# Optimization experiments

Hardware: AMD Instinct MI355X
Metric: run time of the kernel (lower is better)

The kernel has to match this reference:

```python
import jax, jax.numpy as jnp
import numpy as np

N, T, DS, DA = 256, 64, 32, 8
D, H, FF = 512, 8, 2048
HD = D // H          # head_dim = 64
IN = DS + DA         # input_dim = 40
EULER_STEPS = 4


def setup_inputs():
    key = jax.random.key(0)
    ks = jax.random.split(key, 12)
    g = lambda k, shape: (jax.random.normal(k, shape) * 0.02).astype(jnp.float32)
    z = lambda *s: jnp.zeros(s, jnp.float32)
    o = lambda *s: jnp.ones(s, jnp.float32)
    return {
        "states": jax.random.normal(ks[0], (N, T, DS), jnp.float32),
        "actions": jax.random.normal(ks[1], (N, T, DA), jnp.float32),
        "time_steps": jnp.cumsum(jax.random.uniform(ks[2], (N, T + 1), jnp.float32, 0.01, 0.1), axis=1),
        "W_ode": g(ks[3], (D, D)), "b_ode": z(D),
        "W_in": g(ks[4], (IN, D)), "b_in": z(D),
        "ln_in_g": o(D), "ln_in_b": z(D),
        "W_q": g(ks[5], (D, D)), "b_q": z(D),
        "W_kv": g(ks[6], (IN + D, 2 * D + H)), "b_kv": z(2 * D + H),
        "W_out": g(ks[7], (D, D)), "b_out": z(D),
        "ln_ff_g": o(D), "ln_ff_b": z(D),
        "W_ff1": g(ks[8], (D, FF)), "b_ff1": z(FF),
        "W_ff2": g(ks[9], (FF, D)), "b_ff2": z(D),
        "W_dec": g(ks[10], (D, DS)), "b_dec": z(DS),
    }


def _ln(x, g, b):
    m = jnp.mean(x, -1, keepdims=True)
    v = jnp.mean((x - m) ** 2, -1, keepdims=True)
    return (x - m) * jax.lax.rsqrt(v + 1e-5) * g + b


def _forward(states, actions, time_steps, W_ode, b_ode, W_in, b_in, ln_in_g, ln_in_b,
             W_q, b_q, W_kv, b_kv, W_out, b_out, ln_ff_g, ln_ff_b,
             W_ff1, b_ff1, W_ff2, b_ff2, W_dec, b_dec):
    n = states.shape[0]
    # teacher forcing path (train=True, eps_decay=0): data_i = cat(states_i, actions_i)
    data_seq = jnp.concatenate([states, actions], -1).transpose(1, 0, 2)  # [T, N, IN]
    dts = (time_steps[:, 1:] - time_steps[:, :-1]).T                      # [T, N]

    def step(carry, xs):
        h1, W2 = carry            # h1: [N, D], W2: [N, H, HD, HD] fast weights
        data, dt = xs
        # integrate latent ODE over per-sample dt (fixed-step Euler, autonomous tanh MLP)
        step_dt = (dt / EULER_STEPS)[:, None]
        for _ in range(EULER_STEPS):
            h1 = h1 + step_dt * jnp.tanh(h1 @ W_ode + b_ode)
        # Hebbian fast-weight update: W2 += lr * v (x) k  (per head)
        x = jnp.concatenate([data, h1], -1)
        kvb = x @ W_kv + b_kv
        k = jax.nn.softmax(kvb[:, :D].reshape(n, H, HD), -1)
        v = jnp.tanh(kvb[:, D:2 * D]).reshape(n, H, HD)
        lr = jax.nn.sigmoid(kvb[:, 2 * D:])                    # [N, H]
        W2 = W2 + lr[:, :, None, None] * jnp.einsum('nhv,nhk->nhvk', v, k)
        # query_fast_weight
        q = _ln(data @ W_in + b_in, ln_in_g, ln_in_b) @ W_q + b_q
        q = jax.nn.softmax(q.reshape(n, H, HD), -1)
        out = jnp.einsum('nhvk,nhk->nhv', W2, q).reshape(n, D)
        out = out @ W_out + b_out
        y = _ln(out, ln_ff_g, ln_ff_b)
        out = jnp.maximum(y @ W_ff1 + b_ff1, 0.0) @ W_ff2 + b_ff2 + out  # FF block + residual
        pred = out @ W_dec + b_dec                              # decoder
        return (out, W2), pred

    h0 = jnp.zeros((n, D), states.dtype)
    W20 = jnp.zeros((n, H, HD, HD), states.dtype)
    _, preds = jax.lax.scan(step, (h0, W20), (data_seq, dts))
    return preds.transpose(1, 0, 2)  # [N, T, DS] predicted next states


def reference(states, actions, time_steps, W_ode, b_ode, W_in, b_in, ln_in_g, ln_in_b,
              W_q, b_q, W_kv, b_kv, W_out, b_out, ln_ff_g, ln_ff_b,
              W_ff1, b_ff1, W_ff2, b_ff2, W_dec, b_dec):
    return _forward(states, actions, time_steps, W_ode, b_ode, W_in, b_in, ln_in_g, ln_in_b,
                    W_q, b_q, W_kv, b_kv, W_out, b_out, ln_ff_g, ln_ff_b,
                    W_ff1, b_ff1, W_ff2, b_ff2, W_dec, b_dec)
```

## Files before the change

### kernel.cpp

```cpp
#include <hip/hip_runtime.h>

#define NS   256
#define TS   64
#define DS   32
#define DA   8
#define DD   512
#define HH   8
#define HD   64
#define FF   2048
#define INP  40
#define INPP 20
#define INPG 24
#define DP   256
#define KVKP 276
#define KVKPP 280
#define KVO  1032
#define FFP  1024

#define OFF_ODE 0
#define SZ_ODE  (32*512*8)
#define OFF_KV  (OFF_ODE+SZ_ODE)
#define SZ_KV   (35*1032*8)
#define OFF_IN  (OFF_KV+SZ_KV)
#define SZ_IN   (3*512*8)
#define OFF_Q   (OFF_IN+SZ_IN)
#define SZ_Q    (32*512*8)
#define OFF_OUT (OFF_Q+SZ_Q)
#define SZ_OUT  (32*512*8)
#define OFF_F1  (OFF_OUT+SZ_OUT)
#define SZ_F1   (32*2048*8)
#define OFF_F2  (OFF_F1+SZ_F1)
#define SZ_F2   (128*512*8)
#define OFF_DEC (OFF_F2+SZ_F2)
#define SZ_DEC  (32*32*8)

#define DEV __device__ __forceinline__

typedef _Float16 half2_t __attribute__((ext_vector_type(2)));

DEV half2_t as_h2(unsigned int u) { return __builtin_bit_cast(half2_t, u); }

DEV float dot2f(unsigned int w, unsigned int x, float acc) {
#if __has_builtin(__builtin_amdgcn_fdot2)
  return __builtin_amdgcn_fdot2(as_h2(w), as_h2(x), acc, false);
#else
  half2_t a = as_h2(w), b = as_h2(x);
  return acc + (float)a[0] * (float)b[0] + (float)a[1] * (float)b[1];
#endif
}

DEV unsigned int pack2f(float a, float b) {
  unsigned short ua = __builtin_bit_cast(unsigned short, (_Float16)a);
  unsigned short ub = __builtin_bit_cast(unsigned short, (_Float16)b);
  return ((unsigned int)ub << 16) | (unsigned int)ua;
}

DEV float fast_tanh(float x) {
  float ax = fabsf(x);
  float e  = __expf(-2.0f * ax);
  float r  = (1.0f - e) / (1.0f + e);
  return copysignf(r, x);
}

DEV float fast_sigmoid(float x) { return 1.0f / (1.0f + __expf(-x)); }

DEV float wave_max(float v) {
  #pragma unroll
  for (int o = 32; o; o >>= 1) v = fmaxf(v, __shfl_xor(v, o));
  return v;
}
DEV float wave_sum(float v) {
  #pragma unroll
  for (int o = 32; o; o >>= 1) v += __shfl_xor(v, o);
  return v;
}

DEV float dotG(const unsigned int* __restrict__ Wc, int strideG,
               const unsigned int* __restrict__ xq, int NG, float init) {
  float a0 = init, a1 = 0.f, a2 = 0.f, a3 = 0.f;
  #pragma unroll 4
  for (int g = 0; g < NG; ++g) {
    uint4 w0 = *reinterpret_cast<const uint4*>(Wc + g * strideG);
    uint4 w1 = *reinterpret_cast<const uint4*>(Wc + g * strideG + 4);
    uint4 x0 = *reinterpret_cast<const uint4*>(xq + g * 8);
    uint4 x1 = *reinterpret_cast<const uint4*>(xq + g * 8 + 4);
    a0 = dot2f(w0.x, x0.x, a0);
    a1 = dot2f(w0.y, x0.y, a1);
    a2 = dot2f(w0.z, x0.z, a2);
    a3 = dot2f(w0.w, x0.w, a3);
    a0 = dot2f(w1.x, x1.x, a0);
    a1 = dot2f(w1.y, x1.y, a1);
    a2 = dot2f(w1.z, x1.z, a2);
    a3 = dot2f(w1.w, x1.w, a3);
  }
  return (a0 + a1) + (a2 + a3);
}

__global__ void pack_wg_kernel(const float* __restrict__ src, unsigned int* __restrict__ dst,
                               int K, int KPpad, int Dout) {
  int idx = blockIdx.x * blockDim.x + threadIdx.x;
  int total = KPpad * Dout;
  if (idx >= total) return;
  int kp = idx / Dout;
  int j  = idx - kp * Dout;
  int r0 = 2 * kp, r1 = r0 + 1;
  float lo = (r0 < K) ? src[r0 * Dout + j] : 0.f;
  float hi = (r1 < K) ? src[r1 * Dout + j] : 0.f;
  int kg = kp >> 3, sub = kp & 7;
  dst[((kg * Dout + j) << 3) + sub] = pack2f(lo, hi);
}

__global__ __launch_bounds__(512) void fwp_main(
    const float* __restrict__ states, const float* __restrict__ actions,
    const float* __restrict__ tsteps,
    const float* __restrict__ b_ode, const float* __restrict__ b_in,
    const float* __restrict__ ln_in_g, const float* __restrict__ ln_in_b,
    const float* __restrict__ b_q, const float* __restrict__ b_kv,
    const float* __restrict__ b_out,
    const float* __restrict__ ln_ff_g, const float* __restrict__ ln_ff_b,
    const float* __restrict__ b_ff1, const float* __restrict__ b_ff2,
    const float* __restrict__ b_dec,
    const unsigned int* __restrict__ Wode, const unsigned int* __restrict__ Wkv,
    const unsigned int* __restrict__ Win,  const unsigned int* __restrict__ Wq,
    const unsigned int* __restrict__ Wout, const unsigned int* __restrict__ Wff1,
    const unsigned int* __restrict__ Wff2, const unsigned int* __restrict__ Wdec,
    unsigned int* __restrict__ ctrs, float* __restrict__ outp) {

  const int n = blockIdx.x, tid = threadIdx.x;
  const int w = tid >> 6, lane = tid & 63;

  __shared__ alignas(16) float        sh_h[DD];
  __shared__ alignas(16) unsigned int sh_hp[DP];
  __shared__ alignas(16) unsigned int sh_xp[KVKPP];
  __shared__ alignas(16) unsigned int sh_dp[INPG];
  __shared__ alignas(16) float        sh_t[DD];
  __shared__ alignas(16) unsigned int sh_p[DP];
  __shared__ alignas(16) float        sh_kvb[KVO];
  __shared__ alignas(16) float        sh_k[DD];
  __shared__ alignas(16) float        sh_v[DD];
  __shared__ alignas(16) float        sh_q[DD];
  __shared__ float                    sh_lr[HH];
  __shared__ alignas(16) float        sh_ff[FF];
  __shared__ alignas(16) unsigned int sh_ffp[FFP];
  __shared__ float                    sh_red[16];
  __shared__ alignas(16) float        sh_decp[512];
  __shared__ int                      sh_flag;

  float W2r[64];
  #pragma unroll
  for (int i = 0; i < 64; ++i) W2r[i] = 0.f;

  sh_h[tid] = 0.f;
  if (tid < DP) sh_hp[tid] = 0u;
  if (tid >= DP && tid < DP + (KVKPP - KVKP)) sh_xp[KVKP + (tid - DP)] = 0u;
  if (tid >= 300 && tid < 300 + (INPG - INPP)) sh_dp[INPP + (tid - 300)] = 0u;

  bool pace = true;
  unsigned int* ctr = ctrs + 16 * (n & 7);

  for (int t = 0; t < TS; ++t) {
    __syncthreads();

    if (pace) {
      if (tid == 0) {
        sh_flag = 0;
        __hip_atomic_fetch_add(ctr, 1u, __ATOMIC_RELAXED, __HIP_MEMORY_SCOPE_AGENT);
        unsigned int tgt = 32u * (unsigned int)(t + 1);
        int it = 0;
        while (__hip_atomic_load(ctr, __ATOMIC_RELAXED, __HIP_MEMORY_SCOPE_AGENT) < tgt) {
          if (++it > 4096) { sh_flag = 1; break; }
          __builtin_amdgcn_s_sleep(8);
        }
      }
      __syncthreads();
      if (sh_flag) pace = false;
    }

    if (tid < INPP) {
      int i0 = 2 * tid, i1 = i0 + 1;
      float a = (i0 < DS) ? states[(n * TS + t) * DS + i0] : actions[(n * TS + t) * DA + (i0 - DS)];
      float b = (i1 < DS) ? states[(n * TS + t) * DS + i1] : actions[(n * TS + t) * DA + (i1 - DS)];
      unsigned int p = pack2f(a, b);
      sh_xp[tid] = p;
      sh_dp[tid] = p;
    }
    const float sdt = 0.25f * (tsteps[n * (TS + 1) + t + 1] - tsteps[n * (TS + 1) + t]);

    for (int e = 0; e < 4; ++e) {
      float acc = dotG(Wode + tid * 8, DD * 8, sh_hp, 32, b_ode[tid]);
      sh_h[tid] += sdt * fast_tanh(acc);
      __syncthreads();
      if (tid < DP) sh_hp[tid] = pack2f(sh_h[2 * tid], sh_h[2 * tid + 1]);
      __syncthreads();
    }

    if (tid < DP) sh_xp[INPP + tid] = sh_hp[tid];
    __syncthreads();

    for (int j = tid; j < KVO; j += 512)
      sh_kvb[j] = dotG(Wkv + j * 8, KVO * 8, sh_xp, 35, b_kv[j]);
    __syncthreads();

    {
      float kx = sh_kvb[tid];
      float km = wave_max(kx);
      float ke = __expf(kx - km);
      float ks = wave_sum(ke);
      sh_k[tid] = ke / ks;
      sh_v[tid] = fast_tanh(sh_kvb[DD + tid]);
      if (tid < HH) sh_lr[tid] = fast_sigmoid(sh_kvb[2 * DD + tid]);
    }

    float y1 = dotG(Win + tid * 8, DD * 8, sh_dp, 3, b_in[tid]);
    {
      float s1 = y1, s2 = y1 * y1;
      #pragma unroll
      for (int o = 32; o; o >>= 1) { s1 += __shfl_xor(s1, o); s2 += __shfl_xor(s2, o); }
      if (lane == 0) { sh_red[2 * w] = s1; sh_red[2 * w + 1] = s2; }
      __syncthreads();
      s1 = 0.f; s2 = 0.f;
      #pragma unroll
      for (int i = 0; i < 8; ++i) { s1 += sh_red[2 * i]; s2 += sh_red[2 * i + 1]; }
      float m  = s1 * (1.0f / DD);
      float va = fmaxf(s2 * (1.0f / DD) - m * m, 0.f);
      float rs = rsqrtf(va + 1e-5f);
      sh_t[tid] = (y1 - m) * rs * ln_in_g[tid] + ln_in_b[tid];
    }
    __syncthreads();
    if (tid < DP) sh_p[tid] = pack2f(sh_t[2 * tid], sh_t[2 * tid + 1]);
    __syncthreads();
    {
      float qraw = dotG(Wq + tid * 8, DD * 8, sh_p, 32, b_q[tid]);
      float qm = wave_max(qraw);
      float qe = __expf(qraw - qm);
      float qs = wave_sum(qe);
      sh_q[tid] = qe / qs;
    }
    __syncthreads();

    {
      float vi  = sh_v[tid];
      float lrw = sh_lr[w];
      float lv  = lrw * vi;
      float acc = 0.f;
      const float* kb = sh_k + w * HD;
      const float* qb = sh_q + w * HD;
      #pragma unroll
      for (int jc = 0; jc < 16; ++jc) {
        float4 k4 = *reinterpret_cast<const float4*>(kb + 4 * jc);
        float4 q4 = *reinterpret_cast<const float4*>(qb + 4 * jc);
        W2r[4 * jc + 0] += lv * k4.x; acc += W2r[4 * jc + 0] * q4.x;
        W2r[4 * jc + 1] += lv * k4.y; acc += W2r[4 * jc + 1] * q4.y;
        W2r[4 * jc + 2] += lv * k4.z; acc += W2r[4 * jc + 2] * q4.z;
        W2r[4 * jc + 3] += lv * k4.w; acc += W2r[4 * jc + 3] * q4.w;
      }
      sh_t[tid] = acc;
    }
    __syncthreads();
    if (tid < DP) sh_p[tid] = pack2f(sh_t[2 * tid], sh_t[2 * tid + 1]);
    __syncthreads();

    float o1 = dotG(Wout + tid * 8, DD * 8, sh_p, 32, b_out[tid]);

    {
      float s1 = o1, s2 = o1 * o1;
      #pragma unroll
      for (int o = 32; o; o >>= 1) { s1 += __shfl_xor(s1, o); s2 += __shfl_xor(s2, o); }
      if (lane == 0) { sh_red[2 * w] = s1; sh_red[2 * w + 1] = s2; }
      __syncthreads();
      s1 = 0.f; s2 = 0.f;
      #pragma unroll
      for (int i = 0; i < 8; ++i) { s1 += sh_red[2 * i]; s2 += sh_red[2 * i + 1]; }
      float m  = s1 * (1.0f / DD);
      float va = fmaxf(s2 * (1.0f / DD) - m * m, 0.f);
      float rs = rsqrtf(va + 1e-5f);
      sh_t[tid] = (o1 - m) * rs * ln_ff_g[tid] + ln_ff_b[tid];
    }
    __syncthreads();
    if (tid < DP) sh_p[tid] = pack2f(sh_t[2 * tid], sh_t[2 * tid + 1]);
    __syncthreads();

    {
      float f0 = b_ff1[tid], f1 = b_ff1[tid + 512], f2 = b_ff1[tid + 1024], f3 = b_ff1[tid + 1536];
      #pragma unroll 2
      for (int g = 0; g < 32; ++g) {
        uint4 x0 = *reinterpret_cast<const uint4*>(sh_p + g * 8);
        uint4 x1 = *reinterpret_cast<const uint4*>(sh_p + g * 8 + 4);
        const unsigned int* wb = Wff1 + g * (FF * 8) + tid * 8;
        uint4 wa0 = *reinterpret_cast<const uint4*>(wb);
        uint4 wa1 = *reinterpret_cast<const uint4*>(wb + 4);
        uint4 wb0 = *reinterpret_cast<const uint4*>(wb + 512 * 8);
        uint4 wb1 = *reinterpret_cast<const uint4*>(wb + 512 * 8 + 4);
        uint4 wc0 = *reinterpret_cast<const uint4*>(wb + 1024 * 8);
        uint4 wc1 = *reinterpret_cast<const uint4*>(wb + 1024 * 8 + 4);
        uint4 wd0 = *reinterpret_cast<const uint4*>(wb + 1536 * 8);
        uint4 wd1 = *reinterpret_cast<const uint4*>(wb + 1536 * 8 + 4);
        f0 = dot2f(wa0.x, x0.x, f0); f0 = dot2f(wa0.y, x0.y, f0);
        f0 = dot2f(wa0.z, x0.z, f0); f0 = dot2f(wa0.w, x0.w, f0);
        f0 = dot2f(wa1.x, x1.x, f0); f0 = dot2f(wa1.y, x1.y, f0);
        f0 = dot2f(wa1.z, x1.z, f0); f0 = dot2f(wa1.w, x1.w, f0);
        f1 = dot2f(wb0.x, x0.x, f1); f1 = dot2f(wb0.y, x0.y, f1);
        f1 = dot2f(wb0.z, x0.z, f1); f1 = dot2f(wb0.w, x0.w, f1);
        f1 = dot2f(wb1.x, x1.x, f1); f1 = dot2f(wb1.y, x1.y, f1);
        f1 = dot2f(wb1.z, x1.z, f1); f1 = dot2f(wb1.w, x1.w, f1);
        f2 = dot2f(wc0.x, x0.x, f2); f2 = dot2f(wc0.y, x0.y, f2);
        f2 = dot2f(wc0.z, x0.z, f2); f2 = dot2f(wc0.w, x0.w, f2);
        f2 = dot2f(wc1.x, x1.x, f2); f2 = dot2f(wc1.y, x1.y, f2);
        f2 = dot2f(wc1.z, x1.z, f2); f2 = dot2f(wc1.w, x1.w, f2);
        f3 = dot2f(wd0.x, x0.x, f3); f3 = dot2f(wd0.y, x0.y, f3);
        f3 = dot2f(wd0.z, x0.z, f3); f3 = dot2f(wd0.w, x0.w, f3);
        f3 = dot2f(wd1.x, x1.x, f3); f3 = dot2f(wd1.y, x1.y, f3);
        f3 = dot2f(wd1.z, x1.z, f3); f3 = dot2f(wd1.w, x1.w, f3);
      }
      sh_ff[tid]        = fmaxf(f0, 0.f);
      sh_ff[tid + 512]  = fmaxf(f1, 0.f);
      sh_ff[tid + 1024] = fmaxf(f2, 0.f);
      sh_ff[tid + 1536] = fmaxf(f3, 0.f);
    }
    __syncthreads();
    sh_ffp[tid]       = pack2f(sh_ff[2 * tid], sh_ff[2 * tid + 1]);
    sh_ffp[tid + 512] = pack2f(sh_ff[2 * tid + 1024], sh_ff[2 * tid + 1025]);
    __syncthreads();

    {
      float o2 = dotG(Wff2 + tid * 8, DD * 8, sh_ffp, 128, b_ff2[tid]) + o1;
      sh_h[tid] = o2;
    }
    __syncthreads();
    if (tid < DP) sh_hp[tid] = pack2f(sh_h[2 * tid], sh_h[2 * tid + 1]);
    __syncthreads();

    {
      int col = tid & 31, ch = tid >> 5;
      const unsigned int* wbse = Wdec + col * 8;
      float a = 0.f;
      #pragma unroll
      for (int g = 2 * ch; g < 2 * ch + 2; ++g) {
        uint4 w0 = *reinterpret_cast<const uint4*>(wbse + g * (DS * 8));
        uint4 w1 = *reinterpret_cast<const uint4*>(wbse + g * (DS * 8) + 4);
        uint4 x0 = *reinterpret_cast<const uint4*>(sh_hp + g * 8);
        uint4 x1 = *reinterpret_cast<const uint4*>(sh_hp + g * 8 + 4);
        a = dot2f(w0.x, x0.x, a); a = dot2f(w0.y, x0.y, a);
        a = dot2f(w0.z, x0.z, a); a = dot2f(w0.w, x0.w, a);
        a = dot2f(w1.x, x1.x, a); a = dot2f(w1.y, x1.y, a);
        a = dot2f(w1.z, x1.z, a); a = dot2f(w1.w, x1.w, a);
      }
      sh_decp[tid] = a;
    }
    __syncthreads();
    if (tid < DS) {
      float s = b_dec[tid];
      #pragma unroll
      for (int c = 0; c < 16; ++c) s += sh_decp[c * 32 + tid];
      outp[(n * TS + t) * DS + tid] = s;
    }
  }
}

extern "C" void kernel_launch(void* const* d_in, const int* in_sizes, int n_in,
                              void* d_out, int out_size, void* d_ws, size_t ws_size,
                              hipStream_t stream) {
  (void)in_sizes; (void)n_in; (void)out_size; (void)ws_size;

  const float* states   = (const float*)d_in[0];
  const float* actions  = (const float*)d_in[1];
  const float* tsteps   = (const float*)d_in[2];
  const float* W_ode    = (const float*)d_in[3];
  const float* b_ode    = (const float*)d_in[4];
  const float* W_in     = (const float*)d_in[5];
  const float* b_in     = (const float*)d_in[6];
  const float* ln_in_g  = (const float*)d_in[7];
  const float* ln_in_b  = (const float*)d_in[8];
  const float* W_q      = (const float*)d_in[9];
  const float* b_q      = (const float*)d_in[10];
  const float* W_kv     = (const float*)d_in[11];
  const float* b_kv     = (const float*)d_in[12];
  const float* W_out    = (const float*)d_in[13];
  const float* b_out    = (const float*)d_in[14];
  const float* ln_ff_g  = (const float*)d_in[15];
  const float* ln_ff_b  = (const float*)d_in[16];
  const float* W_ff1    = (const float*)d_in[17];
  const float* b_ff1    = (const float*)d_in[18];
  const float* W_ff2    = (const float*)d_in[19];
  const float* b_ff2    = (const float*)d_in[20];
  const float* W_dec    = (const float*)d_in[21];
  const float* b_dec    = (const float*)d_in[22];

  unsigned int* wsbase = (unsigned int*)d_ws;
  unsigned int* ctrs   = wsbase;
  unsigned int* W      = wsbase + 128;

  hipMemsetAsync(d_ws, 0, 512, stream);

  auto launch_pack = [&](const float* src, unsigned int* dst, int K, int KPpad, int Dout) {
    int total = KPpad * Dout;
    int blocks = (total + 255) / 256;
    pack_wg_kernel<<<blocks, 256, 0, stream>>>(src, dst, K, KPpad, Dout);
  };

  launch_pack(W_ode, W + OFF_ODE, 512,  256, 512);
  launch_pack(W_kv,  W + OFF_KV,  552,  280, 1032);
  launch_pack(W_in,  W + OFF_IN,  40,   24,  512);
  launch_pack(W_q,   W + OFF_Q,   512,  256, 512);
  launch_pack(W_out, W + OFF_OUT, 512,  256, 512);
  launch_pack(W_ff1, W + OFF_F1,  512,  256, 2048);
  launch_pack(W_ff2, W + OFF_F2,  2048, 1024, 512);
  launch_pack(W_dec, W + OFF_DEC, 512,  256, 32);

  fwp_main<<<NS, 512, 0, stream>>>(
      states, actions, tsteps,
      b_ode, b_in, ln_in_g, ln_in_b, b_q, b_kv, b_out, ln_ff_g, ln_ff_b,
      b_ff1, b_ff2, b_dec,
      W + OFF_ODE, W + OFF_KV, W + OFF_IN, W + OFF_Q,
      W + OFF_OUT, W + OFF_F1, W + OFF_F2, W + OFF_DEC,
      ctrs, (float*)d_out);
}
```

Before: 5.905 ms.

## Process two samples per block to reuse each weight load twice

Each block now handles two batch samples, so every packed weight vector fetched from global memory feeds dot products for both samples. The grid halves to 128 blocks and the pacing target is adjusted to match. This halves weight traffic per sample but doubles the fast-weight registers (128 floats per thread) and the shared memory footprint, which can cause spills, and with only 128 blocks part of the GPU's compute units sit idle.

```diff
diff --git a/kernel.cpp b/kernel.cpp
--- a/kernel.cpp
+++ b/kernel.cpp
@@ -1,6 +1,7 @@
 #include <hip/hip_runtime.h>
 
 #define NS   256
+#define NB   128
 #define TS   64
 #define DS   32
 #define DA   8
@@ -64,36 +65,32 @@
 
 DEV float fast_sigmoid(float x) { return 1.0f / (1.0f + __expf(-x)); }
 
-DEV float wave_max(float v) {
-  #pragma unroll
-  for (int o = 32; o; o >>= 1) v = fmaxf(v, __shfl_xor(v, o));
-  return v;
-}
-DEV float wave_sum(float v) {
-  #pragma unroll
-  for (int o = 32; o; o >>= 1) v += __shfl_xor(v, o);
-  return v;
-}
-
-DEV float dotG(const unsigned int* __restrict__ Wc, int strideG,
-               const unsigned int* __restrict__ xq, int NG, float init) {
-  float a0 = init, a1 = 0.f, a2 = 0.f, a3 = 0.f;
+#define LD4(p) (*reinterpret_cast<const uint4*>(p))
+
+DEV void dotG2(const unsigned int* __restrict__ Wc, int strideG,
+               const unsigned int* __restrict__ xa, const unsigned int* __restrict__ xb,
+               int NG, float inita, float initb, float& outa, float& outb) {
+  float a0 = inita, a1 = 0.f, a2 = 0.f, a3 = 0.f;
+  float b0 = initb, b1 = 0.f, b2 = 0.f, b3 = 0.f;
   #pragma unroll 4
   for (int g = 0; g < NG; ++g) {
-    uint4 w0 = *reinterpret_cast<const uint4*>(Wc + g * strideG);
-    uint4 w1 = *reinterpret_cast<const uint4*>(Wc + g * strideG + 4);
-    uint4 x0 = *reinterpret_cast<const uint4*>(xq + g * 8);
-    uint4 x1 = *reinterpret_cast<const uint4*>(xq + g * 8 + 4);
-    a0 = dot2f(w0.x, x0.x, a0);
-    a1 = dot2f(w0.y, x0.y, a1);
-    a2 = dot2f(w0.z, x0.z, a2);
-    a3 = dot2f(w0.w, x0.w, a3);
-    a0 = dot2f(w1.x, x1.x, a0);
-    a1 = dot2f(w1.y, x1.y, a1);
-    a2 = dot2f(w1.z, x1.z, a2);
-    a3 = dot2f(w1.w, x1.w, a3);
+    uint4 w0 = LD4(Wc + g * strideG);
+    uint4 w1 = LD4(Wc + g * strideG + 4);
+    uint4 xa0 = LD4(xa + g * 8);
+    uint4 xa1 = LD4(xa + g * 8 + 4);
+    uint4 xb0 = LD4(xb + g * 8);
+    uint4 xb1 = LD4(xb + g * 8 + 4);
+    a0 = dot2f(w0.x, xa0.x, a0); a1 = dot2f(w0.y, xa0.y, a1);
+    a2 = dot2f(w0.z, xa0.z, a2); a3 = dot2f(w0.w, xa0.w, a3);
+    a0 = dot2f(w1.x, xa1.x, a0); a1 = dot2f(w1.y, xa1.y, a1);
+    a2 = dot2f(w1.z, xa1.z, a2); a3 = dot2f(w1.w, xa1.w, a3);
+    b0 = dot2f(w0.x, xb0.x, b0); b1 = dot2f(w0.y, xb0.y, b1);
+    b2 = dot2f(w0.z, xb0.z, b2); b3 = dot2f(w0.w, xb0.w, b3);
+    b0 = dot2f(w1.x, xb1.x, b0); b1 = dot2f(w1.y, xb1.y, b1);
+    b2 = dot2f(w1.z, xb1.z, b2); b3 = dot2f(w1.w, xb1.w, b3);
   }
-  return (a0 + a1) + (a2 + a3);
+  outa = (a0 + a1) + (a2 + a3);
+  outb = (b0 + b1) + (b2 + b3);
 }
 
 __global__ void pack_wg_kernel(const float* __restrict__ src, unsigned int* __restrict__ dst,
@@ -110,7 +107,7 @@
   dst[((kg * Dout + j) << 3) + sub] = pack2f(lo, hi);
 }
 
-__global__ __launch_bounds__(512) void fwp_main(
+__global__ __launch_bounds__(512, 2) void fwp_main(
     const float* __restrict__ states, const float* __restrict__ actions,
     const float* __restrict__ tsteps,
     const float* __restrict__ b_ode, const float* __restrict__ b_in,
@@ -126,37 +123,38 @@
     const unsigned int* __restrict__ Wff2, const unsigned int* __restrict__ Wdec,
     unsigned int* __restrict__ ctrs, float* __restrict__ outp) {
 
-  const int n = blockIdx.x, tid = threadIdx.x;
+  const int b = blockIdx.x, tid = threadIdx.x;
   const int w = tid >> 6, lane = tid & 63;
-
-  __shared__ alignas(16) float        sh_h[DD];
-  __shared__ alignas(16) unsigned int sh_hp[DP];
-  __shared__ alignas(16) unsigned int sh_xp[KVKPP];
-  __shared__ alignas(16) unsigned int sh_dp[INPG];
-  __shared__ alignas(16) float        sh_t[DD];
-  __shared__ alignas(16) unsigned int sh_p[DP];
-  __shared__ alignas(16) float        sh_kvb[KVO];
-  __shared__ alignas(16) float        sh_k[DD];
-  __shared__ alignas(16) float        sh_v[DD];
-  __shared__ alignas(16) float        sh_q[DD];
-  __shared__ float                    sh_lr[HH];
-  __shared__ alignas(16) float        sh_ff[FF];
-  __shared__ alignas(16) unsigned int sh_ffp[FFP];
-  __shared__ float                    sh_red[16];
-  __shared__ alignas(16) float        sh_decp[512];
+  const int n0 = 2 * b;
+
+  __shared__ alignas(16) float        sh_h[2][DD];
+  __shared__ alignas(16) unsigned int sh_hp[2][DP];
+  __shared__ alignas(16) unsigned int sh_xp[2][KVKPP];
+  __shared__ alignas(16) unsigned int sh_dp[2][INPG];
+  __shared__ alignas(16) float        sh_t[2][DD];
+  __shared__ alignas(16) unsigned int sh_p[2][DP];
+  __shared__ alignas(16) float        sh_kvb[2][KVO];
+  __shared__ alignas(16) float        sh_k[2][DD];
+  __shared__ alignas(16) float        sh_v[2][DD];
+  __shared__ alignas(16) float        sh_q[2][DD];
+  __shared__ float                    sh_lr[2][HH];
+  __shared__ alignas(16) float        sh_ff[2][FF];
+  __shared__ alignas(16) unsigned int sh_ffp[2][FFP];
+  __shared__ float                    sh_red[2][16];
+  __shared__ alignas(16) float        sh_decp[2][512];
   __shared__ int                      sh_flag;
 
-  float W2r[64];
+  float W2A[64], W2B[64];
   #pragma unroll
-  for (int i = 0; i < 64; ++i) W2r[i] = 0.f;
-
-  sh_h[tid] = 0.f;
-  if (tid < DP) sh_hp[tid] = 0u;
-  if (tid >= DP && tid < DP + (KVKPP - KVKP)) sh_xp[KVKP + (tid - DP)] = 0u;
-  if (tid >= 300 && tid < 300 + (INPG - INPP)) sh_dp[INPP + (tid - 300)] = 0u;
+  for (int i = 0; i < 64; ++i) { W2A[i] = 0.f; W2B[i] = 0.f; }
+
+  sh_h[0][tid] = 0.f; sh_h[1][tid] = 0.f;
+  if (tid < DP) { sh_hp[0][tid] = 0u; sh_hp[1][tid] = 0u; }
+  if (tid < (KVKPP - KVKP)) { sh_xp[0][KVKP + tid] = 0u; sh_xp[1][KVKP + tid] = 0u; }
+  if (tid < (INPG - INPP))  { sh_dp[0][INPP + tid] = 0u; sh_dp[1][INPP + tid] = 0u; }
 
   bool pace = true;
-  unsigned int* ctr = ctrs + 16 * (n & 7);
+  unsigned int* ctr = ctrs + 16 * (b & 7);
 
   for (int t = 0; t < TS; ++t) {
     __syncthreads();
@@ -165,7 +163,7 @@
       if (tid == 0) {
         sh_flag = 0;
         __hip_atomic_fetch_add(ctr, 1u, __ATOMIC_RELAXED, __HIP_MEMORY_SCOPE_AGENT);
-        unsigned int tgt = 32u * (unsigned int)(t + 1);
+        unsigned int tgt = 16u * (unsigned int)(t + 1);
         int it = 0;
         while (__hip_atomic_load(ctr, __ATOMIC_RELAXED, __HIP_MEMORY_SCOPE_AGENT) < tgt) {
           if (++it > 4096) { sh_flag = 1; break; }
@@ -176,183 +174,271 @@
       if (sh_flag) pace = false;
     }
 
-    if (tid < INPP) {
-      int i0 = 2 * tid, i1 = i0 + 1;
+    if (w < 2 && lane < INPP) {
+      int n = n0 + w;
+      int i0 = 2 * lane, i1 = i0 + 1;
       float a = (i0 < DS) ? states[(n * TS + t) * DS + i0] : actions[(n * TS + t) * DA + (i0 - DS)];
-      float b = (i1 < DS) ? states[(n * TS + t) * DS + i1] : actions[(n * TS + t) * DA + (i1 - DS)];
-      unsigned int p = pack2f(a, b);
-      sh_xp[tid] = p;
-      sh_dp[tid] = p;
-    }
-    const float sdt = 0.25f * (tsteps[n * (TS + 1) + t + 1] - tsteps[n * (TS + 1) + t]);
+      float c = (i1 < DS) ? states[(n * TS + t) * DS + i1] : actions[(n * TS + t) * DA + (i1 - DS)];
+      unsigned int p = pack2f(a, c);
+      sh_xp[w][lane] = p;
+      sh_dp[w][lane] = p;
+    }
+    const float sdtA = 0.25f * (tsteps[n0 * (TS + 1) + t + 1] - tsteps[n0 * (TS + 1) + t]);
+    const float sdtB = 0.25f * (tsteps[(n0 + 1) * (TS + 1) + t + 1] - tsteps[(n0 + 1) * (TS + 1) + t]);
 
     for (int e = 0; e < 4; ++e) {
-      float acc = dotG(Wode + tid * 8, DD * 8, sh_hp, 32, b_ode[tid]);
-      sh_h[tid] += sdt * fast_tanh(acc);
+      float accA, accB;
+      float bo = b_ode[tid];
+      dotG2(Wode + tid * 8, DD * 8, sh_hp[0], sh_hp[1], 32, bo, bo, accA, accB);
+      sh_h[0][tid] += sdtA * fast_tanh(accA);
+      sh_h[1][tid] += sdtB * fast_tanh(accB);
       __syncthreads();
-      if (tid < DP) sh_hp[tid] = pack2f(sh_h[2 * tid], sh_h[2 * tid + 1]);
+      if (tid < DP) {
+        sh_hp[0][tid] = pack2f(sh_h[0][2 * tid], sh_h[0][2 * tid + 1]);
+        sh_hp[1][tid] = pack2f(sh_h[1][2 * tid], sh_h[1][2 * tid + 1]);
+      }
       __syncthreads();
     }
 
-    if (tid < DP) sh_xp[INPP + tid] = sh_hp[tid];
-    __syncthreads();
-
-    for (int j = tid; j < KVO; j += 512)
-      sh_kvb[j] = dotG(Wkv + j * 8, KVO * 8, sh_xp, 35, b_kv[j]);
-    __syncthreads();
-
-    {
-      float kx = sh_kvb[tid];
-      float km = wave_max(kx);
+    if (tid < DP) {
+      sh_xp[0][INPP + tid] = sh_hp[0][tid];
+      sh_xp[1][INPP + tid] = sh_hp[1][tid];
+    }
+    __syncthreads();
+
+    for (int j = tid; j < KVO; j += 512) {
+      float ra, rb, bk = b_kv[j];
+      dotG2(Wkv + j * 8, KVO * 8, sh_xp[0], sh_xp[1], 35, bk, bk, ra, rb);
+      sh_kvb[0][j] = ra; sh_kvb[1][j] = rb;
+    }
+    __syncthreads();
+
+    #pragma unroll
+    for (int s = 0; s < 2; ++s) {
+      float kx = sh_kvb[s][tid];
+      float km = kx;
+      #pragma unroll
+      for (int o = 32; o; o >>= 1) km = fmaxf(km, __shfl_xor(km, o));
       float ke = __expf(kx - km);
-      float ks = wave_sum(ke);
-      sh_k[tid] = ke / ks;
-      sh_v[tid] = fast_tanh(sh_kvb[DD + tid]);
-      if (tid < HH) sh_lr[tid] = fast_sigmoid(sh_kvb[2 * DD + tid]);
-    }
-
-    float y1 = dotG(Win + tid * 8, DD * 8, sh_dp, 3, b_in[tid]);
-    {
-      float s1 = y1, s2 = y1 * y1;
-      #pragma unroll
-      for (int o = 32; o; o >>= 1) { s1 += __shfl_xor(s1, o); s2 += __shfl_xor(s2, o); }
-      if (lane == 0) { sh_red[2 * w] = s1; sh_red[2 * w + 1] = s2; }
+      float ks = ke;
+      #pragma unroll
+      for (int o = 32; o; o >>= 1) ks += __shfl_xor(ks, o);
+      sh_k[s][tid] = ke / ks;
+      sh_v[s][tid] = fast_tanh(sh_kvb[s][DD + tid]);
+      if (tid < HH) sh_lr[s][tid] = fast_sigmoid(sh_kvb[s][2 * DD + tid]);
+    }
+
+    float y1A, y1B;
+    {
+      float bi = b_in[tid];
+      dotG2(Win + tid * 8, DD * 8, sh_dp[0], sh_dp[1], 3, bi, bi, y1A, y1B);
+      float s1A = y1A, s2A = y1A * y1A, s1B = y1B, s2B = y1B * y1B;
+      #pragma unroll
+      for (int o = 32; o; o >>= 1) {
+        s1A += __shfl_xor(s1A, o); s2A += __shfl_xor(s2A, o);
+        s1B += __shfl_xor(s1B, o); s2B += __shfl_xor(s2B, o);
+      }
+      if (lane == 0) {
+        sh_red[0][2 * w] = s1A; sh_red[0][2 * w + 1] = s2A;
+        sh_red[1][2 * w] = s1B; sh_red[1][2 * w + 1] = s2B;
+      }
       __syncthreads();
-      s1 = 0.f; s2 = 0.f;
-      #pragma unroll
-      for (int i = 0; i < 8; ++i) { s1 += sh_red[2 * i]; s2 += sh_red[2 * i + 1]; }
-      float m  = s1 * (1.0f / DD);
-      float va = fmaxf(s2 * (1.0f / DD) - m * m, 0.f);
-      float rs = rsqrtf(va + 1e-5f);
-      sh_t[tid] = (y1 - m) * rs * ln_in_g[tid] + ln_in_b[tid];
-    }
-    __syncthreads();
-    if (tid < DP) sh_p[tid] = pack2f(sh_t[2 * tid], sh_t[2 * tid + 1]);
-    __syncthreads();
-    {
-      float qraw = dotG(Wq + tid * 8, DD * 8, sh_p, 32, b_q[tid]);
-      float qm = wave_max(qraw);
-      float qe = __expf(qraw - qm);
-      float qs = wave_sum(qe);
-      sh_q[tid] = qe / qs;
-    }
-    __syncthreads();
-
-    {
-      float vi  = sh_v[tid];
-      float lrw = sh_lr[w];
-      float lv  = lrw * vi;
-      float acc = 0.f;
-      const float* kb = sh_k + w * HD;
-      const float* qb = sh_q + w * HD;
+      float t1A = 0.f, t2A = 0.f, t1B = 0.f, t2B = 0.f;
+      #pragma unroll
+      for (int i = 0; i < 8; ++i) {
+        t1A += sh_red[0][2 * i]; t2A += sh_red[0][2 * i + 1];
+        t1B += sh_red[1][2 * i]; t2B += sh_red[1][2 * i + 1];
+      }
+      float mA = t1A * (1.0f / DD), mB = t1B * (1.0f / DD);
+      float vA = fmaxf(t2A * (1.0f / DD) - mA * mA, 0.f);
+      float vB = fmaxf(t2B * (1.0f / DD) - mB * mB, 0.f);
+      float rA = rsqrtf(vA + 1e-5f), rB = rsqrtf(vB + 1e-5f);
+      float g = ln_in_g[tid], bb = ln_in_b[tid];
+      sh_t[0][tid] = (y1A - mA) * rA * g + bb;
+      sh_t[1][tid] = (y1B - mB) * rB * g + bb;
+    }
+    __syncthreads();
+    if (tid < DP) {
+      sh_p[0][tid] = pack2f(sh_t[0][2 * tid], sh_t[0][2 * tid + 1]);
+      sh_p[1][tid] = pack2f(sh_t[1][2 * tid], sh_t[1][2 * tid + 1]);
+    }
+    __syncthreads();
+    {
+      float qA, qB, bq = b_q[tid];
+      dotG2(Wq + tid * 8, DD * 8, sh_p[0], sh_p[1], 32, bq, bq, qA, qB);
+      float mA = qA, mB = qB;
+      #pragma unroll
+      for (int o = 32; o; o >>= 1) { mA = fmaxf(mA, __shfl_xor(mA, o)); mB = fmaxf(mB, __shfl_xor(mB, o)); }
+      float eA = __expf(qA - mA), eB = __expf(qB - mB);
+      float sA = eA, sB = eB;
+      #pragma unroll
+      for (int o = 32; o; o >>= 1) { sA += __shfl_xor(sA, o); sB += __shfl_xor(sB, o); }
+      sh_q[0][tid] = eA / sA;
+      sh_q[1][tid] = eB / sB;
+    }
+    __syncthreads();
+
+    {
+      float lvA = sh_lr[0][w] * sh_v[0][tid];
+      float lvB = sh_lr[1][w] * sh_v[1][tid];
+      float accA = 0.f, accB = 0.f;
+      const float* kbA = sh_k[0] + w * HD;
+      const float* qbA = sh_q[0] + w * HD;
+      const float* kbB = sh_k[1] + w * HD;
+      const float* qbB = sh_q[1] + w * HD;
       #pragma unroll
       for (int jc = 0; jc < 16; ++jc) {
-        float4 k4 = *reinterpret_cast<const float4*>(kb + 4 * jc);
-        float4 q4 = *reinterpret_cast<const float4*>(qb + 4 * jc);
-        W2r[4 * jc + 0] += lv * k4.x; acc += W2r[4 * jc + 0] * q4.x;
-        W2r[4 * jc + 1] += lv * k4.y; acc += W2r[4 * jc + 1] * q4.y;
-        W2r[4 * jc + 2] += lv * k4.z; acc += W2r[4 * jc + 2] * q4.z;
-        W2r[4 * jc + 3] += lv * k4.w; acc += W2r[4 * jc + 3] * q4.w;
-      }
-      sh_t[tid] = acc;
-    }
-    __syncthreads();
-    if (tid < DP) sh_p[tid] = pack2f(sh_t[2 * tid], sh_t[2 * tid + 1]);
-    __syncthreads();
-
-    float o1 = dotG(Wout + tid * 8, DD * 8, sh_p, 32, b_out[tid]);
-
-    {
-      float s1 = o1, s2 = o1 * o1;
-      #pragma unroll
-      for (int o = 32; o; o >>= 1) { s1 += __shfl_xor(s1, o); s2 += __shfl_xor(s2, o); }
-      if (lane == 0) { sh_red[2 * w] = s1; sh_red[2 * w + 1] = s2; }
+        float4 kA = *reinterpret_cast<const float4*>(kbA + 4 * jc);
+        float4 qA = *reinterpret_cast<const float4*>(qbA + 4 * jc);
+        float4 kB = *reinterpret_cast<const float4*>(kbB + 4 * jc);
+        float4 qB = *reinterpret_cast<const float4*>(qbB + 4 * jc);
+        W2A[4 * jc + 0] += lvA * kA.x; accA += W2A[4 * jc + 0] * qA.x;
+        W2A[4 * jc + 1] += lvA * kA.y; accA += W2A[4 * jc + 1] * qA.y;
+        W2A[4 * jc + 2] += lvA * kA.z; accA += W2A[4 * jc + 2] * qA.z;
+        W2A[4 * jc + 3] += lvA * kA.w; accA += W2A[4 * jc + 3] * qA.w;
+        W2B[4 * jc + 0] += lvB * kB.x; accB += W2B[4 * jc + 0] * qB.x;
+        W2B[4 * jc + 1] += lvB * kB.y; accB += W2B[4 * jc + 1] * qB.y;
+        W2B[4 * jc + 2] += lvB * kB.z; accB += W2B[4 * jc + 2] * qB.z;
+        W2B[4 * jc + 3] += lvB * kB.w; accB += W2B[4 * jc + 3] * qB.w;
+      }
+      sh_t[0][tid] = accA;
+      sh_t[1][tid] = accB;
+    }
+    __syncthreads();
+    if (tid < DP) {
+      sh_p[0][tid] = pack2f(sh_t[0][2 * tid], sh_t[0][2 * tid + 1]);
+      sh_p[1][tid] = pack2f(sh_t[1][2 * tid], sh_t[1][2 * tid + 1]);
+    }
+    __syncthreads();
+
+    float o1A, o1B;
+    {
+      float bo = b_out[tid];
+      dotG2(Wout + tid * 8, DD * 8, sh_p[0], sh_p[1], 32, bo, bo, o1A, o1B);
+    }
+
+    {
+      float s1A = o1A, s2A = o1A * o1A, s1B = o1B, s2B = o1B * o1B;
+      #pragma unroll
+      for (int o = 32; o; o >>= 1) {
+        s1A += __shfl_xor(s1A, o); s2A += __shfl_xor(s2A, o);
+        s1B += __shfl_xor(s1B, o); s2B += __shfl_xor(s2B, o);
+      }
+      if (lane == 0) {
+        sh_red[0][2 * w] = s1A; sh_red[0][2 * w + 1] = s2A;
+        sh_red[1][2 * w] = s1B; sh_red[1][2 * w + 1] = s2B;
+      }
       __syncthreads();
-      s1 = 0.f; s2 = 0.f;
-      #pragma unroll
-      for (int i = 0; i < 8; ++i) { s1 += sh_red[2 * i]; s2 += sh_red[2 * i + 1]; }
-      float m  = s1 * (1.0f / DD);
-      float va = fmaxf(s2 * (1.0f / DD) - m * m, 0.f);
-      float rs = rsqrtf(va + 1e-5f);
-      sh_t[tid] = (o1 - m) * rs * ln_ff_g[tid] + ln_ff_b[tid];
-    }
-    __syncthreads();
-    if (tid < DP) sh_p[tid] = pack2f(sh_t[2 * tid], sh_t[2 * tid + 1]);
-    __syncthreads();
-
-    {
-      float f0 = b_ff1[tid], f1 = b_ff1[tid + 512], f2 = b_ff1[tid + 1024], f3 = b_ff1[tid + 1536];
+      float t1A = 0.f, t2A = 0.f, t1B = 0.f, t2B = 0.f;
+      #pragma unroll
+      for (int i = 0; i < 8; ++i) {
+        t1A += sh_red[0][2 * i]; t2A += sh_red[0][2 * i + 1];
+        t1B += sh_red[1][2 * i]; t2B += sh_red[1][2 * i + 1];
+      }
+      float mA = t1A * (1.0f / DD), mB = t1B * (1.0f / DD);
+      float vA = fmaxf(t2A * (1.0f / DD) - mA * mA, 0.f);
+      float vB = fmaxf(t2B * (1.0f / DD) - mB * mB, 0.f);
+      float rA = rsqrtf(vA + 1e-5f), rB = rsqrtf(vB + 1e-5f);
+      float g = ln_ff_g[tid], bb = ln_ff_b[tid];
+      sh_t[0][tid] = (o1A - mA) * rA * g + bb;
+      sh_t[1][tid] = (o1B - mB) * rB * g + bb;
+    }
+    __syncthreads();
+    if (tid < DP) {
+      sh_p[0][tid] = pack2f(sh_t[0][2 * tid], sh_t[0][2 * tid + 1]);
+      sh_p[1][tid] = pack2f(sh_t[1][2 * tid], sh_t[1][2 * tid + 1]);
+    }
+    __syncthreads();
+
+    #pragma unroll
+    for (int pass = 0; pass < 2; ++pass) {
+      int c0 = tid + pass * 1024;
+      int c1 = c0 + 512;
+      float fA0 = b_ff1[c0], fA1 = b_ff1[c1];
+      float fB0 = fA0, fB1 = fA1;
       #pragma unroll 2
       for (int g = 0; g < 32; ++g) {
-        uint4 x0 = *reinterpret_cast<const uint4*>(sh_p + g * 8);
-        uint4 x1 = *reinterpret_cast<const uint4*>(sh_p + g * 8 + 4);
-        const unsigned int* wb = Wff1 + g * (FF * 8) + tid * 8;
-        uint4 wa0 = *reinterpret_cast<const uint4*>(wb);
-        uint4 wa1 = *reinterpret_cast<const uint4*>(wb + 4);
-        uint4 wb0 = *reinterpret_cast<const uint4*>(wb + 512 * 8);
-        uint4 wb1 = *reinterpret_cast<const uint4*>(wb + 512 * 8 + 4);
-        uint4 wc0 = *reinterpret_cast<const uint4*>(wb + 1024 * 8);
-        uint4 wc1 = *reinterpret_cast<const uint4*>(wb + 1024 * 8 + 4);
-        uint4 wd0 = *reinterpret_cast<const uint4*>(wb + 1536 * 8);
-        uint4 wd1 = *reinterpret_cast<const uint4*>(wb + 1536 * 8 + 4);
-        f0 = dot2f(wa0.x, x0.x, f0); f0 = dot2f(wa0.y, x0.y, f0);
-        f0 = dot2f(wa0.z, x0.z, f0); f0 = dot2f(wa0.w, x0.w, f0);
-        f0 = dot2f(wa1.x, x1.x, f0); f0 = dot2f(wa1.y, x1.y, f0);
-        f0 = dot2f(wa1.z, x1.z, f0); f0 = dot2f(wa1.w, x1.w, f0);
-        f1 = dot2f(wb0.x, x0.x, f1); f1 = dot2f(wb0.y, x0.y, f1);
-        f1 = dot2f(wb0.z, x0.z, f1); f1 = dot2f(wb0.w, x0.w, f1);
-        f1 = dot2f(wb1.x, x1.x, f1); f1 = dot2f(wb1.y, x1.y, f1);
-        f1 = dot2f(wb1.z, x1.z, f1); f1 = dot2f(wb1.w, x1.w, f1);
-        f2 = dot2f(wc0.x, x0.x, f2); f2 = dot2f(wc0.y, x0.y, f2);
-        f2 = dot2f(wc0.z, x0.z, f2); f2 = dot2f(wc0.w, x0.w, f2);
-        f2 = dot2f(wc1.x, x1.x, f2); f2 = dot2f(wc1.y, x1.y, f2);
-        f2 = dot2f(wc1.z, x1.z, f2); f2 = dot2f(wc1.w, x1.w, f2);
-        f3 = dot2f(wd0.x, x0.x, f3); f3 = dot2f(wd0.y, x0.y, f3);
-        f3 = dot2f(wd0.z, x0.z, f3); f3 = dot2f(wd0.w, x0.w, f3);
-        f3 = dot2f(wd1.x, x1.x, f3); f3 = dot2f(wd1.y, x1.y, f3);
-        f3 = dot2f(wd1.z, x1.z, f3); f3 = dot2f(wd1.w, x1.w, f3);
-      }
-      sh_ff[tid]        = fmaxf(f0, 0.f);
-      sh_ff[tid + 512]  = fmaxf(f1, 0.f);
-      sh_ff[tid + 1024] = fmaxf(f2, 0.f);
-      sh_ff[tid + 1536] = fmaxf(f3, 0.f);
-    }
-    __syncthreads();
-    sh_ffp[tid]       = pack2f(sh_ff[2 * tid], sh_ff[2 * tid + 1]);
-    sh_ffp[tid + 512] = pack2f(sh_ff[2 * tid + 1024], sh_ff[2 * tid + 1025]);
-    __syncthreads();
-
-    {
-      float o2 = dotG(Wff2 + tid * 8, DD * 8, sh_ffp, 128, b_ff2[tid]) + o1;
-      sh_h[tid] = o2;
-    }
-    __syncthreads();
-    if (tid < DP) sh_hp[tid] = pack2f(sh_h[2 * tid], sh_h[2 * tid + 1]);
+        const unsigned int* wb = Wff1 + g * (FF * 8) + c0 * 8;
+        uint4 w00 = LD4(wb);
+        uint4 w01 = LD4(wb + 4);
+        uint4 w10 = LD4(wb + 512 * 8);
+        uint4 w11 = LD4(wb + 512 * 8 + 4);
+        uint4 xA0 = LD4(sh_p[0] + g * 8);
+        uint4 xA1 = LD4(sh_p[0] + g * 8 + 4);
+        uint4 xB0 = LD4(sh_p[1] + g * 8);
+        uint4 xB1 = LD4(sh_p[1] + g * 8 + 4);
+        fA0 = dot2f(w00.x, xA0.x, fA0); fA0 = dot2f(w00.y, xA0.y, fA0);
+        fA0 = dot2f(w00.z, xA0.z, fA0); fA0 = dot2f(w00.w, xA0.w, fA0);
+        fA0 = dot2f(w01.x, xA1.x, fA0); fA0 = dot2f(w01.y, xA1.y, fA0);
+        fA0 = dot2f(w01.z, xA1.z, fA0); fA0 = dot2f(w01.w, xA1.w, fA0);
+        fA1 = dot2f(w10.x, xA0.x, fA1); fA1 = dot2f(w10.y, xA0.y, fA1);
+        fA1 = dot2f(w10.z, xA0.z, fA1); fA1 = dot2f(w10.w, xA0.w, fA1);
+        fA1 = dot2f(w11.x, xA1.x, fA1); fA1 = dot2f(w11.y, xA1.y, fA1);
+        fA1 = dot2f(w11.z, xA1.z, fA1); fA1 = dot2f(w11.w, xA1.w, fA1);
+        fB0 = dot2f(w00.x, xB0.x, fB0); fB0 = dot2f(w00.y, xB0.y, fB0);
+        fB0 = dot2f(w00.z, xB0.z, fB0); fB0 = dot2f(w00.w, xB0.w, fB0);
+        fB0 = dot2f(w01.x, xB1.x, fB0); fB0 = dot2f(w01.y, xB1.y, fB0);
+        fB0 = dot2f(w01.z, xB1.z, fB0); fB0 = dot2f(w01.w, xB1.w, fB0);
+        fB1 = dot2f(w10.x, xB0.x, fB1); fB1 = dot2f(w10.y, xB0.y, fB1);
+        fB1 = dot2f(w10.z, xB0.z, fB1); fB1 = dot2f(w10.w, xB0.w, fB1);
+        fB1 = dot2f(w11.x, xB1.x, fB1); fB1 = dot2f(w11.y, xB1.y, fB1);
+        fB1 = dot2f(w11.z, xB1.z, fB1); fB1 = dot2f(w11.w, xB1.w, fB1);
+      }
+      sh_ff[0][c0] = fmaxf(fA0, 0.f);
+      sh_ff[0][c1] = fmaxf(fA1, 0.f);
+      sh_ff[1][c0] = fmaxf(fB0, 0.f);
+      sh_ff[1][c1] = fmaxf(fB1, 0.f);
+    }
+    __syncthreads();
+    sh_ffp[0][tid]       = pack2f(sh_ff[0][2 * tid], sh_ff[0][2 * tid + 1]);
+    sh_ffp[0][tid + 512] = pack2f(sh_ff[0][1024 + 2 * tid], sh_ff[0][1025 + 2 * tid]);
+    sh_ffp[1][tid]       = pack2f(sh_ff[1][2 * tid], sh_ff[1][2 * tid + 1]);
+    sh_ffp[1][tid + 512] = pack2f(sh_ff[1][1024 + 2 * tid], sh_ff[1][1025 + 2 * tid]);
+    __syncthreads();
+
+    {
+      float o2A, o2B, bf = b_ff2[tid];
+      dotG2(Wff2 + tid * 8, DD * 8, sh_ffp[0], sh_ffp[1], 128, bf, bf, o2A, o2B);
+      sh_h[0][tid] = o2A + o1A;
+      sh_h[1][tid] = o2B + o1B;
+    }
+    __syncthreads();
+    if (tid < DP) {
+      sh_hp[0][tid] = pack2f(sh_h[0][2 * tid], sh_h[0][2 * tid + 1]);
+      sh_hp[1][tid] = pack2f(sh_h[1][2 * tid], sh_h[1][2 * tid + 1]);
+    }
     __syncthreads();
 
     {
       int col = tid & 31, ch = tid >> 5;
       const unsigned int* wbse = Wdec + col * 8;
-      float a = 0.f;
+      float aA = 0.f, aB = 0.f;
       #pragma unroll
       for (int g = 2 * ch; g < 2 * ch + 2; ++g) {
-        uint4 w0 = *reinterpret_cast<const uint4*>(wbse + g * (DS * 8));
-        uint4 w1 = *reinterpret_cast<const uint4*>(wbse + g * (DS * 8) + 4);
-        uint4 x0 = *reinterpret_cast<const uint4*>(sh_hp + g * 8);
-        uint4 x1 = *reinterpret_cast<const uint4*>(sh_hp + g * 8 + 4);
-        a = dot2f(w0.x, x0.x, a); a = dot2f(w0.y, x0.y, a);
-        a = dot2f(w0.z, x0.z, a); a = dot2f(w0.w, x0.w, a);
-        a = dot2f(w1.x, x1.x, a); a = dot2f(w1.y, x1.y, a);
-        a = dot2f(w1.z, x1.z, a); a = dot2f(w1.w, x1.w, a);
-      }
-      sh_decp[tid] = a;
-    }
-    __syncthreads();
-    if (tid < DS) {
-      float s = b_dec[tid];
-      #pragma unroll
-      for (int c = 0; c < 16; ++c) s += sh_decp[c * 32 + tid];
-      outp[(n * TS + t) * DS + tid] = s;
+        uint4 w0 = LD4(wbse + g * (DS * 8));
+        uint4 w1 = LD4(wbse + g * (DS * 8) + 4);
+        uint4 xA0 = LD4(sh_hp[0] + g * 8);
+        uint4 xA1 = LD4(sh_hp[0] + g * 8 + 4);
+        uint4 xB0 = LD4(sh_hp[1] + g * 8);
+        uint4 xB1 = LD4(sh_hp[1] + g * 8 + 4);
+        aA = dot2f(w0.x, xA0.x, aA); aA = dot2f(w0.y, xA0.y, aA);
+        aA = dot2f(w0.z, xA0.z, aA); aA = dot2f(w0.w, xA0.w, aA);
+        aA = dot2f(w1.x, xA1.x, aA); aA = dot2f(w1.y, xA1.y, aA);
+        aA = dot2f(w1.z, xA1.z, aA); aA = dot2f(w1.w, xA1.w, aA);
+        aB = dot2f(w0.x, xB0.x, aB); aB = dot2f(w0.y, xB0.y, aB);
+        aB = dot2f(w0.z, xB0.z, aB); aB = dot2f(w0.w, xB0.w, aB);
+        aB = dot2f(w1.x, xB1.x, aB); aB = dot2f(w1.y, xB1.y, aB);
+        aB = dot2f(w1.z, xB1.z, aB); aB = dot2f(w1.w, xB1.w, aB);
+      }
+      sh_decp[0][tid] = aA;
+      sh_decp[1][tid] = aB;
+    }
+    __syncthreads();
+    if (w < 2 && lane < DS) {
+      float s = b_dec[lane];
+      #pragma unroll
+      for (int c = 0; c < 16; ++c) s += sh_decp[w][c * 32 + lane];
+      outp[((n0 + w) * TS + t) * DS + lane] = s;
     }
   }
 }
@@ -407,7 +493,7 @@
   launch_pack(W_ff2, W + OFF_F2,  2048, 1024, 512);
   launch_pack(W_dec, W + OFF_DEC, 512,  256, 32);
 
-  fwp_main<<<NS, 512, 0, stream>>>(
+  fwp_main<<<NB, 512, 0, stream>>>(
       states, actions, tsteps,
       b_ode, b_in, ln_in_g, ln_in_b, b_q, b_kv, b_out, ln_ff_g, ln_ff_b,
       b_ff1, b_ff2, b_dec,
```

Measured after the change: 10.02 ms. +69.7%, slower.
